# Performance work log

Measured on AMD Instinct MI355X. Metric: run time of the kernel, lower is better.

The kernel has to match this reference:

```python
import jax, jax.numpy as jnp
import numpy as np
from jax import lax

B, S, D, H, FF, STEPS = 8, 1024, 512, 8, 2048, 64
HD = D // H
EPS = 1e-5
NEG_INF = -1e30


def setup_inputs() -> dict:
    key = jax.random.key(0)
    ks = jax.random.split(key, 8)
    sc = 0.02
    inp = {
        "x": jax.random.normal(ks[0], (B, S, D), jnp.float32),
        "decode_x": jax.random.normal(ks[1], (STEPS, B, 1, D), jnp.float32),
        # bool attn mask, True = masked (future positions), matching the torch code
        "causal_mask": jnp.triu(jnp.ones((S, S), bool), k=1),
        "qkv_w": jax.random.normal(ks[2], (3 * D, D), jnp.float32) * sc,
        "qkv_b": jnp.zeros((3 * D,), jnp.float32),
        "out_w": jax.random.normal(ks[3], (D, D), jnp.float32) * sc,
        "out_b": jnp.zeros((D,), jnp.float32),
        "w1": jax.random.normal(ks[4], (FF, D), jnp.float32) * sc,
        "b1": jnp.zeros((FF,), jnp.float32),
        "w2": jax.random.normal(ks[5], (D, FF), jnp.float32) * sc,
        "b2": jnp.zeros((D,), jnp.float32),
        "ln1_w": jnp.ones((D,), jnp.float32),
        "ln1_b": jnp.zeros((D,), jnp.float32),
        "ln2_w": jnp.ones((D,), jnp.float32),
        "ln2_b": jnp.zeros((D,), jnp.float32),
    }
    return inp


def _layer_norm(x, w, b):
    mu = jnp.mean(x, axis=-1, keepdims=True)
    var = jnp.mean(jnp.square(x - mu), axis=-1, keepdims=True)
    return (x - mu) * lax.rsqrt(var + EPS) * w + b


def _mlp(x, w1, b1, w2, b2):
    h = jax.nn.relu(jnp.einsum("bsd,fd->bsf", x, w1) + b1)
    return jnp.einsum("bsf,df->bsd", h, w2) + b2


def _attend(q, k, v, mask):
    # q:[B,H,L,hd] k,v:[B,H,T,hd] mask broadcastable to [B,H,L,T], True = masked
    scale = 1.0 / np.sqrt(HD)
    scores = jnp.einsum("bhld,bhtd->bhlt", q, k) * scale
    scores = jnp.where(mask, NEG_INF, scores)
    w = jax.nn.softmax(scores, axis=-1)
    w = jnp.where(mask, 0.0, w)  # torch code zeros masked weights post-softmax
    return jnp.einsum("bhlt,bhtd->bhld", w, v)


def _heads(t):  # [B,T,D] -> [B,H,T,hd]
    return t.reshape(t.shape[0], t.shape[1], H, HD).transpose(0, 2, 1, 3)


def reference(x, decode_x, causal_mask, qkv_w, qkv_b, out_w, out_b,
              w1, b1, w2, b2, ln1_w, ln1_b, ln2_w, ln2_b):
    # ---- process_prompt (prefill) ----
    qkv = jnp.einsum("bsd,ed->bse", x, qkv_w) + qkv_b  # [B,S,3D]
    q, k, v = jnp.split(qkv, 3, axis=-1)
    attn = _attend(_heads(q), _heads(k), _heads(v), causal_mask[None, None])
    attn = attn.transpose(0, 2, 1, 3).reshape(B, S, D)
    h = x + (jnp.einsum("bsd,ed->bse", attn, out_w) + out_b)
    h = _layer_norm(h, ln1_w, ln1_b)
    h = h + _mlp(h, w1, b1, w2, b2)
    prefill_out = _layer_norm(h, ln2_w, ln2_b)

    cap = S + STEPS
    k_cache = jnp.zeros((B, cap, D), x.dtype).at[:, :S].set(k)
    v_cache = jnp.zeros((B, cap, D), x.dtype).at[:, :S].set(v)
    pos = jnp.arange(cap)

    def step(carry, x_t):
        k_cache, v_cache, cur_len = carry
        qkv = jnp.einsum("bsd,ed->bse", x_t, qkv_w) + qkv_b  # [B,1,3D]
        q, kk, vv = jnp.split(qkv, 3, axis=-1)
        k_cache = lax.dynamic_update_slice(k_cache, kk, (0, cur_len, 0))
        v_cache = lax.dynamic_update_slice(v_cache, vv, (0, cur_len, 0))
        kv_len = cur_len + 1
        mask = (pos >= kv_len)[None, None, None, :]  # [1,1,1,cap]
        attn = _attend(_heads(q), _heads(k_cache), _heads(v_cache), mask)
        attn = attn.transpose(0, 2, 1, 3).reshape(B, 1, D)
        h = x_t + (jnp.einsum("bsd,ed->bse", attn, out_w) + out_b)
        h = _layer_norm(h, ln1_w, ln1_b)
        h = h + _mlp(h, w1, b1, w2, b2)
        h = _layer_norm(h, ln2_w, ln2_b)
        return (k_cache, v_cache, kv_len), h

    (_, _, _), dec = lax.scan(step, (k_cache, v_cache, jnp.int32(S)), decode_x)
    dec = dec.squeeze(2).transpose(1, 0, 2)  # [B,STEPS,D]
    return jnp.concatenate([prefill_out, dec], axis=1)  # [B,S+STEPS,D]
```

## Files before the change

kernel.cpp:

```cpp
#include <hip/hip_runtime.h>
#include <cstdint>

#define CAP_ 1088
#define EPS_ 1e-5f

using bf8   = __attribute__((ext_vector_type(8))) short;
using f32x4 = __attribute__((ext_vector_type(4))) float;

__device__ __forceinline__ unsigned short f2bf(float f) {
  unsigned u = __float_as_uint(f);
  u += 0x7fffu + ((u >> 16) & 1);
  return (unsigned short)(u >> 16);
}

typedef const __attribute__((address_space(1))) void* gp1;
typedef __attribute__((address_space(3))) void* lp3;
__device__ __forceinline__ void async16(const void* g, void* l) {
  __builtin_amdgcn_global_load_lds((gp1)g, (lp3)l, 16, 0, 0);
}

__global__ __launch_bounds__(256) void cvt_bf16(const float* __restrict__ in,
                                                unsigned short* __restrict__ out,
                                                int n4) {
  int i = blockIdx.x * 256 + threadIdx.x;
  if (i >= n4) return;
  float4 v = ((const float4*)in)[i];
  ushort4 o;
  o.x = f2bf(v.x); o.y = f2bf(v.y); o.z = f2bf(v.z); o.w = f2bf(v.w);
  ((ushort4*)out)[i] = o;
}

__global__ __launch_bounds__(256) void mfma_gemm(
    const unsigned short* __restrict__ A, const unsigned short* __restrict__ Bw,
    const float* __restrict__ bias, const float* __restrict__ res,
    const float* __restrict__ res2,
    float* __restrict__ Cf, unsigned short* __restrict__ Cb,
    unsigned short* __restrict__ kb, unsigned short* __restrict__ vt,
    int M, int N, int K, int mode, int relu)
{
  __shared__ unsigned short Als[128 * 64];
  __shared__ unsigned short Bls[128 * 64];
  const int tid  = threadIdx.x;
  const int lane = tid & 63, w = tid >> 6;
  const int bm = blockIdx.x * 128, bn = blockIdx.y * 128;
  const int wm = (w >> 1) * 64, wn = (w & 1) * 64;

  f32x4 acc[4][4] = {};

  const int so = tid * 16;
  for (int k0 = 0; k0 < K; k0 += 64) {
#pragma unroll
    for (int it = 0; it < 4; ++it) {
      int o   = it * 4096 + so;
      int row = o >> 7;
      int ch  = (o >> 4) & 7;
      int sch = ch ^ (row & 7);
      async16(A  + (size_t)(bm + row) * K + k0 + sch * 8, (char*)Als + o);
      async16(Bw + (size_t)(bn + row) * K + k0 + sch * 8, (char*)Bls + o);
    }
    __syncthreads();
#pragma unroll
    for (int ks = 0; ks < 2; ++ks) {
      bf8 af[4], bfr[4];
#pragma unroll
      for (int m = 0; m < 4; ++m) {
        int row = wm + m * 16 + (lane & 15);
        int ch  = ks * 4 + (lane >> 4);
        af[m] = *(const bf8*)((const char*)Als + row * 128 + ((ch ^ (row & 7)) * 16));
      }
#pragma unroll
      for (int n = 0; n < 4; ++n) {
        int row = wn + n * 16 + (lane & 15);
        int ch  = ks * 4 + (lane >> 4);
        bfr[n] = *(const bf8*)((const char*)Bls + row * 128 + ((ch ^ (row & 7)) * 16));
      }
#pragma unroll
      for (int m = 0; m < 4; ++m)
#pragma unroll
        for (int n = 0; n < 4; ++n)
          acc[m][n] = __builtin_amdgcn_mfma_f32_16x16x32_bf16(af[m], bfr[n], acc[m][n], 0, 0, 0);
    }
    __syncthreads();
  }

#pragma unroll
  for (int m = 0; m < 4; ++m) {
#pragma unroll
    for (int n = 0; n < 4; ++n) {
      int col  = bn + wn + n * 16 + (lane & 15);
      int row0 = bm + wm + m * 16 + ((lane >> 4) << 2);
      float bcol = bias[col];
      if (mode == 1) {
        if (col < 512) {
#pragma unroll
          for (int r = 0; r < 4; ++r)
            Cb[((size_t)(row0 + r) << 9) + col] = f2bf((acc[m][n][r] + bcol) * 0.125f);
        } else if (col < 1024) {
#pragma unroll
          for (int r = 0; r < 4; ++r) {
            int row = row0 + r; int bb, pos;
            if (row < 8192) { bb = row >> 10; pos = row & 1023; }
            else { int r2 = row - 8192; bb = r2 & 7; pos = 1024 + (r2 >> 3); }
            kb[(((size_t)(bb * CAP_ + pos)) << 9) + (col - 512)] = f2bf(acc[m][n][r] + bcol);
          }
        } else {
          int c = col - 1024; int hh = c >> 6, d = c & 63;
          if (row0 < 8192) {
            int bb = row0 >> 10, pos = row0 & 1023;
            ushort4 pk;
            pk.x = f2bf(acc[m][n][0] + bcol); pk.y = f2bf(acc[m][n][1] + bcol);
            pk.z = f2bf(acc[m][n][2] + bcol); pk.w = f2bf(acc[m][n][3] + bcol);
            *(ushort4*)(vt + ((size_t)((bb * 8 + hh) * 64 + d)) * CAP_ + pos) = pk;
          } else {
#pragma unroll
            for (int r = 0; r < 4; ++r) {
              int r2 = row0 + r - 8192; int bb = r2 & 7, pos = 1024 + (r2 >> 3);
              vt[((size_t)((bb * 8 + hh) * 64 + d)) * CAP_ + pos] = f2bf(acc[m][n][r] + bcol);
            }
          }
        }
      } else {
#pragma unroll
        for (int r = 0; r < 4; ++r) {
          int row = row0 + r;
          float v = acc[m][n][r] + bcol;
          if (relu) v = fmaxf(v, 0.f);
          if (res) {
            if (res2 && row >= 8192) v += res2[((size_t)(row - 8192) << 9) + col];
            else                     v += res[(size_t)row * N + col];
          }
          if (mode == 0) Cf[(size_t)row * N + col] = v;
          else           Cb[(size_t)row * N + col] = f2bf(v);
        }
      }
    }
  }
}

__global__ __launch_bounds__(256) void attn_mfma(
    const unsigned short* __restrict__ qb,
    const unsigned short* __restrict__ kcb,
    const unsigned short* __restrict__ vtb,
    unsigned short* __restrict__ ob)
{
  __shared__ unsigned short Kls[4096];
  __shared__ unsigned short Vls[4096];
  __shared__ unsigned short Pls[4096];
  const int st = blockIdx.x, bh = blockIdx.y;
  const int b = bh >> 3, h = bh & 7;
  const bool dec = (st == 16);
  const int tid = threadIdx.x, lane = tid & 63, w = tid >> 6;
  const int wq = w * 16;
  const int nT = dec ? 17 : st + 1;
  const int qi = wq + (lane & 15);
  const size_t g = dec ? (size_t)(8192 + qi * 8 + b)
                       : (size_t)((b << 10) + st * 64 + qi);

  const bf8 qf0 = *(const bf8*)(qb + (g << 9) + h * 64 +      ((lane >> 4) << 3));
  const bf8 qf1 = *(const bf8*)(qb + (g << 9) + h * 64 + 32 + ((lane >> 4) << 3));

  f32x4 oo[4] = {};
  float m_ = -1e30f, l_ = 0.f;

  const size_t kbase = (((size_t)b * CAP_) << 9) + h * 64;
  const size_t vbase = (size_t)((b * 8 + h) * 64) * CAP_;

  for (int t = 0; t < nT; ++t) {
    const int t0 = t * 64;
    __syncthreads();
#pragma unroll
    for (int it = 0; it < 2; ++it) {
      int o   = it * 4096 + tid * 16;
      int row = o >> 7;
      int sch = ((o >> 4) & 7) ^ (row & 7);
      async16(kcb + kbase + (((size_t)(t0 + row)) << 9) + sch * 8, (char*)Kls + o);
      async16(vtb + vbase + (size_t)row * CAP_ + t0 + sch * 8,     (char*)Vls + o);
    }
    __syncthreads();

    f32x4 sfr[4] = {};
#pragma unroll
    for (int ks = 0; ks < 2; ++ks) {
      int cb = ks * 4 + (lane >> 4);
      bf8 qv = ks ? qf1 : qf0;
#pragma unroll
      for (int f = 0; f < 4; ++f) {
        int row = f * 16 + (lane & 15);
        bf8 kf = *(const bf8*)((const char*)Kls + row * 128 + ((cb ^ (row & 7)) << 4));
        sfr[f] = __builtin_amdgcn_mfma_f32_16x16x32_bf16(kf, qv, sfr[f], 0, 0, 0);
      }
    }
    if (t == nT - 1) {
#pragma unroll
      for (int f = 0; f < 4; ++f)
#pragma unroll
        for (int r = 0; r < 4; ++r) {
          int tr = f * 16 + ((lane >> 4) << 2) + r;
          if (tr > qi) sfr[f][r] = -1e30f;
        }
    }

    float pmax = -1e30f;
#pragma unroll
    for (int f = 0; f < 4; ++f)
#pragma unroll
      for (int r = 0; r < 4; ++r) pmax = fmaxf(pmax, sfr[f][r]);
    pmax = fmaxf(pmax, __shfl_xor(pmax, 16, 64));
    pmax = fmaxf(pmax, __shfl_xor(pmax, 32, 64));
    float mn  = fmaxf(m_, pmax);
    float fsc = __expf(m_ - mn);
    float rs = 0.f;
#pragma unroll
    for (int f = 0; f < 4; ++f)
#pragma unroll
      for (int r = 0; r < 4; ++r) {
        float e = __expf(sfr[f][r] - mn);
        sfr[f][r] = e; rs += e;
      }
    rs += __shfl_xor(rs, 16, 64);
    rs += __shfl_xor(rs, 32, 64);
    l_ = l_ * fsc + rs; m_ = mn;
#pragma unroll
    for (int f = 0; f < 4; ++f) oo[f] *= fsc;

#pragma unroll
    for (int f = 0; f < 4; ++f) {
      ushort4 pk;
      pk.x = f2bf(sfr[f][0]); pk.y = f2bf(sfr[f][1]);
      pk.z = f2bf(sfr[f][2]); pk.w = f2bf(sfr[f][3]);
      int tb   = f * 32 + ((lane >> 4) << 3);
      int addr = qi * 128 + ((((tb >> 4)) ^ (qi & 7)) << 4) + (tb & 15);
      *(ushort4*)((char*)Pls + addr) = pk;
    }
    __syncthreads();

#pragma unroll
    for (int ks = 0; ks < 2; ++ks) {
      int cb = ks * 4 + (lane >> 4);
      bf8 pf = *(const bf8*)((const char*)Pls + qi * 128 + ((cb ^ (qi & 7)) << 4));
#pragma unroll
      for (int f = 0; f < 4; ++f) {
        int row = f * 16 + (lane & 15);
        bf8 vf = *(const bf8*)((const char*)Vls + row * 128 + ((cb ^ (row & 7)) << 4));
        oo[f] = __builtin_amdgcn_mfma_f32_16x16x32_bf16(vf, pf, oo[f], 0, 0, 0);
      }
    }
  }

  const float inv = 1.f / l_;
#pragma unroll
  for (int f = 0; f < 4; ++f) {
    ushort4 pk;
    pk.x = f2bf(oo[f][0] * inv); pk.y = f2bf(oo[f][1] * inv);
    pk.z = f2bf(oo[f][2] * inv); pk.w = f2bf(oo[f][3] * inv);
    int d0 = f * 16 + ((lane >> 4) << 2);
    *(ushort4*)(ob + (g << 9) + h * 64 + d0) = pk;
  }
}

__global__ __launch_bounds__(256) void ln_rows(
    const float* __restrict__ in, float* __restrict__ outf,
    unsigned short* __restrict__ outb,
    const float* __restrict__ w, const float* __restrict__ bb,
    int outmode)
{
  __shared__ float s1[256], s2[256];
  const int m = blockIdx.x, tid = threadIdx.x;
  const float* row = in + ((size_t)m << 9);
  float x0 = row[tid], x1 = row[tid + 256];
  s1[tid] = x0 + x1;
  s2[tid] = x0 * x0 + x1 * x1;
  __syncthreads();
  for (int st = 128; st > 0; st >>= 1) {
    if (tid < st) { s1[tid] += s1[tid + st]; s2[tid] += s2[tid + st]; }
    __syncthreads();
  }
  float mu  = s1[0] * (1.f / 512.f);
  float var = s2[0] * (1.f / 512.f) - mu * mu;
  float inv = rsqrtf(var + EPS_);
  size_t ob;
  if (outmode == 0) ob = (size_t)m << 9;
  else {
    int b, s;
    if (m < 8192) { b = m >> 10; s = m & 1023; }
    else { int r2 = m - 8192; b = r2 & 7; s = 1024 + (r2 >> 3); }
    ob = ((size_t)(b * CAP_ + s)) << 9;
  }
  float y0 = (x0 - mu) * inv * w[tid] + bb[tid];
  float y1 = (x1 - mu) * inv * w[tid + 256] + bb[tid + 256];
  outf[ob + tid] = y0; outf[ob + tid + 256] = y1;
  if (outb) {
    outb[((size_t)m << 9) + tid]       = f2bf(y0);
    outb[((size_t)m << 9) + tid + 256] = f2bf(y1);
  }
}

extern "C" void kernel_launch(void* const* d_in, const int* in_sizes, int n_in,
                              void* d_out, int out_size, void* d_ws, size_t ws_size,
                              hipStream_t stream)
{
  const float* x     = (const float*)d_in[0];
  const float* dx    = (const float*)d_in[1];
  const float* qkv_w = (const float*)d_in[3];
  const float* qkv_b = (const float*)d_in[4];
  const float* out_w = (const float*)d_in[5];
  const float* out_b = (const float*)d_in[6];
  const float* w1    = (const float*)d_in[7];
  const float* b1    = (const float*)d_in[8];
  const float* w2    = (const float*)d_in[9];
  const float* b2    = (const float*)d_in[10];
  const float* ln1w  = (const float*)d_in[11];
  const float* ln1b  = (const float*)d_in[12];
  const float* ln2w  = (const float*)d_in[13];
  const float* ln2b  = (const float*)d_in[14];
  float* out = (float*)d_out;

  float* ws = (float*)d_ws;
  size_t o = 0;
  unsigned short* x_bf    = (unsigned short*)(ws + o); o += (size_t)8704 * 256;
  unsigned short* qkvw_bf = (unsigned short*)(ws + o); o += 1536 * 256;
  unsigned short* outw_bf = (unsigned short*)(ws + o); o += 512 * 256;
  unsigned short* w1_bf   = (unsigned short*)(ws + o); o += 2048 * 256;
  unsigned short* w2_bf   = (unsigned short*)(ws + o); o += (size_t)512 * 1024;
  unsigned short* qb_bf   = (unsigned short*)(ws + o); o += (size_t)8704 * 256;
  unsigned short* kcb     = (unsigned short*)(ws + o); o += (size_t)8 * CAP_ * 256;
  unsigned short* vtb     = (unsigned short*)(ws + o); o += (size_t)8 * 512 * CAP_ / 2;
  unsigned short* attn_bf = (unsigned short*)(ws + o); o += (size_t)8704 * 256;
  float* h                = ws + o;                    o += (size_t)8704 * 512;
  unsigned short* h_bf    = (unsigned short*)(ws + o); o += (size_t)8704 * 256;
  unsigned short* hid_bf  = (unsigned short*)(ws + o); o += (size_t)8704 * 1024;
  float* h2               = ws + o;                    o += (size_t)8704 * 512;

  cvt_bf16<<<dim3(4096), 256, 0, stream>>>(x,  x_bf,                      1048576);
  cvt_bf16<<<dim3(256),  256, 0, stream>>>(dx, x_bf + (size_t)8192 * 512, 65536);
  cvt_bf16<<<dim3(768),  256, 0, stream>>>(qkv_w, qkvw_bf, 196608);
  cvt_bf16<<<dim3(256),  256, 0, stream>>>(out_w, outw_bf, 65536);
  cvt_bf16<<<dim3(1024), 256, 0, stream>>>(w1,    w1_bf,   262144);
  cvt_bf16<<<dim3(1024), 256, 0, stream>>>(w2,    w2_bf,   262144);

  mfma_gemm<<<dim3(68, 12), 256, 0, stream>>>(x_bf, qkvw_bf, qkv_b, nullptr, nullptr,
      nullptr, qb_bf, kcb, vtb, 8704, 1536, 512, 1, 0);
  attn_mfma<<<dim3(17, 64), 256, 0, stream>>>(qb_bf, kcb, vtb, attn_bf);
  mfma_gemm<<<dim3(68, 4), 256, 0, stream>>>(attn_bf, outw_bf, out_b, x, dx,
      h, nullptr, nullptr, nullptr, 8704, 512, 512, 0, 0);
  ln_rows<<<dim3(8704), 256, 0, stream>>>(h, h, h_bf, ln1w, ln1b, 0);
  mfma_gemm<<<dim3(68, 16), 256, 0, stream>>>(h_bf, w1_bf, b1, nullptr, nullptr,
      nullptr, hid_bf, nullptr, nullptr, 8704, 2048, 512, 2, 1);
  mfma_gemm<<<dim3(68, 4), 256, 0, stream>>>(hid_bf, w2_bf, b2, h, nullptr,
      h2, nullptr, nullptr, nullptr, 8704, 512, 2048, 0, 0);
  ln_rows<<<dim3(8704), 256, 0, stream>>>(h2, out, nullptr, ln2w, ln2b, 5);
}
```

Before: 350.1 us.

## Fuse residual add and LayerNorm into full-row output-projection and FFN2 GEMMs

Adds a GEMM kernel where each block computes 32 full rows of 512 outputs, so bias, residual add and LayerNorm run in the epilogue, replacing the separate ln_rows launches and fp32 intermediates. Residuals are now read from bf16 copies (x_bf, h1_bf) rather than fp32, which cuts memory traffic but lowers the precision of the residual path. The new kernel uses 272 blocks with 64KB LDS and no double buffering of B, so it may get less parallelism than the previous 68x4 tiling.

```diff
diff --git a/kernel.cpp b/kernel.cpp
--- a/kernel.cpp
+++ b/kernel.cpp
@@ -11,6 +11,9 @@
   unsigned u = __float_as_uint(f);
   u += 0x7fffu + ((u >> 16) & 1);
   return (unsigned short)(u >> 16);
+}
+__device__ __forceinline__ float bf2f(unsigned short v) {
+  return __uint_as_float((unsigned)v << 16);
 }
 
 typedef const __attribute__((address_space(1))) void* gp1;
@@ -32,9 +35,8 @@
 
 __global__ __launch_bounds__(256) void mfma_gemm(
     const unsigned short* __restrict__ A, const unsigned short* __restrict__ Bw,
-    const float* __restrict__ bias, const float* __restrict__ res,
-    const float* __restrict__ res2,
-    float* __restrict__ Cf, unsigned short* __restrict__ Cb,
+    const float* __restrict__ bias,
+    unsigned short* __restrict__ Cb,
     unsigned short* __restrict__ kb, unsigned short* __restrict__ vt,
     int M, int N, int K, int mode, int relu)
 {
@@ -122,19 +124,143 @@
       } else {
 #pragma unroll
         for (int r = 0; r < 4; ++r) {
-          int row = row0 + r;
           float v = acc[m][n][r] + bcol;
           if (relu) v = fmaxf(v, 0.f);
-          if (res) {
-            if (res2 && row >= 8192) v += res2[((size_t)(row - 8192) << 9) + col];
-            else                     v += res[(size_t)row * N + col];
-          }
-          if (mode == 0) Cf[(size_t)row * N + col] = v;
-          else           Cb[(size_t)row * N + col] = f2bf(v);
+          Cb[(size_t)(row0 + r) * N + col] = f2bf(v);
         }
       }
     }
   }
+}
+
+__global__ __launch_bounds__(256) void gemm_fullrow_ln(
+    const unsigned short* __restrict__ A,
+    const unsigned short* __restrict__ Bw,
+    const float* __restrict__ bias,
+    const unsigned short* __restrict__ resb,
+    const float* __restrict__ lnw, const float* __restrict__ lnb,
+    unsigned short* __restrict__ outb, float* __restrict__ outf,
+    int K, int mode)
+{
+  __shared__ unsigned short Bls[512 * 64];
+  const int tid = threadIdx.x, lane = tid & 63, w = tid >> 6;
+  const int l4 = lane >> 4, l15 = lane & 15;
+  const int bm = blockIdx.x * 32;
+
+  f32x4 acc[2][8] = {};
+  bf8 a_cur[2][2], a_nxt[2][2];
+
+#pragma unroll
+  for (int ks = 0; ks < 2; ++ks)
+#pragma unroll
+    for (int mf = 0; mf < 2; ++mf)
+      a_cur[ks][mf] = *(const bf8*)(A + (size_t)(bm + mf * 16 + l15) * K + (ks * 4 + l4) * 8);
+
+  for (int k0 = 0; k0 < K; k0 += 64) {
+#pragma unroll
+    for (int it = 0; it < 16; ++it) {
+      int o   = it * 4096 + tid * 16;
+      int row = o >> 7;
+      int sch = ((o >> 4) & 7) ^ (row & 7);
+      async16(Bw + (size_t)row * K + k0 + sch * 8, (char*)Bls + o);
+    }
+    if (k0 + 64 < K) {
+#pragma unroll
+      for (int ks = 0; ks < 2; ++ks)
+#pragma unroll
+        for (int mf = 0; mf < 2; ++mf)
+          a_nxt[ks][mf] = *(const bf8*)(A + (size_t)(bm + mf * 16 + l15) * K +
+                                        k0 + 64 + (ks * 4 + l4) * 8);
+    }
+    __syncthreads();
+#pragma unroll
+    for (int ks = 0; ks < 2; ++ks) {
+      int cb = ks * 4 + l4;
+#pragma unroll
+      for (int nf = 0; nf < 8; ++nf) {
+        int row = w * 128 + nf * 16 + l15;
+        bf8 bfv = *(const bf8*)((const char*)Bls + row * 128 + ((cb ^ (row & 7)) << 4));
+#pragma unroll
+        for (int mf = 0; mf < 2; ++mf)
+          acc[mf][nf] = __builtin_amdgcn_mfma_f32_16x16x32_bf16(a_cur[ks][mf], bfv, acc[mf][nf], 0, 0, 0);
+      }
+    }
+#pragma unroll
+    for (int ks = 0; ks < 2; ++ks)
+#pragma unroll
+      for (int mf = 0; mf < 2; ++mf)
+        a_cur[ks][mf] = a_nxt[ks][mf];
+    __syncthreads();
+  }
+
+  float bc[8], lw[8], lb[8];
+#pragma unroll
+  for (int nf = 0; nf < 8; ++nf) {
+    int col = w * 128 + nf * 16 + l15;
+    bc[nf] = bias[col]; lw[nf] = lnw[col]; lb[nf] = lnb[col];
+  }
+#pragma unroll
+  for (int nf = 0; nf < 8; ++nf) {
+    int col = w * 128 + nf * 16 + l15;
+#pragma unroll
+    for (int mf = 0; mf < 2; ++mf)
+#pragma unroll
+      for (int r = 0; r < 4; ++r) {
+        int rowg = bm + mf * 16 + l4 * 4 + r;
+        acc[mf][nf][r] += bc[nf] + bf2f(resb[(size_t)rowg * 512 + col]);
+      }
+  }
+
+  float* red = (float*)Bls;
+#pragma unroll
+  for (int mf = 0; mf < 2; ++mf)
+#pragma unroll
+    for (int r = 0; r < 4; ++r) {
+      float s = 0.f, q = 0.f;
+#pragma unroll
+      for (int nf = 0; nf < 8; ++nf) { float v = acc[mf][nf][r]; s += v; q += v * v; }
+#pragma unroll
+      for (int off = 1; off < 16; off <<= 1) {
+        s += __shfl_xor(s, off, 64); q += __shfl_xor(q, off, 64);
+      }
+      if (l15 == 0) {
+        int rl = mf * 16 + l4 * 4 + r;
+        red[rl * 8 + w * 2]     = s;
+        red[rl * 8 + w * 2 + 1] = q;
+      }
+    }
+  __syncthreads();
+
+#pragma unroll
+  for (int mf = 0; mf < 2; ++mf)
+#pragma unroll
+    for (int r = 0; r < 4; ++r) {
+      int rl = mf * 16 + l4 * 4 + r;
+      float S = red[rl * 8 + 0] + red[rl * 8 + 2] + red[rl * 8 + 4] + red[rl * 8 + 6];
+      float Q = red[rl * 8 + 1] + red[rl * 8 + 3] + red[rl * 8 + 5] + red[rl * 8 + 7];
+      float mu  = S * (1.f / 512.f);
+      float var = Q * (1.f / 512.f) - mu * mu;
+      float inv = rsqrtf(var + EPS_);
+      int rowg = bm + rl;
+      if (mode == 0) {
+#pragma unroll
+        for (int nf = 0; nf < 8; ++nf) {
+          int col = w * 128 + nf * 16 + l15;
+          float y = (acc[mf][nf][r] - mu) * inv * lw[nf] + lb[nf];
+          outb[(size_t)rowg * 512 + col] = f2bf(y);
+        }
+      } else {
+        int b, s2;
+        if (rowg < 8192) { b = rowg >> 10; s2 = rowg & 1023; }
+        else { int r2 = rowg - 8192; b = r2 & 7; s2 = 1024 + (r2 >> 3); }
+        size_t ob = ((size_t)(b * CAP_ + s2)) << 9;
+#pragma unroll
+        for (int nf = 0; nf < 8; ++nf) {
+          int col = w * 128 + nf * 16 + l15;
+          outf[ob + col] = (acc[mf][nf][r] - mu) * inv * lw[nf] + lb[nf];
+        }
+      }
+    }
 }
 
 __global__ __launch_bounds__(256) void attn_mfma(
@@ -255,43 +381,6 @@
     pk.z = f2bf(oo[f][2] * inv); pk.w = f2bf(oo[f][3] * inv);
     int d0 = f * 16 + ((lane >> 4) << 2);
     *(ushort4*)(ob + (g << 9) + h * 64 + d0) = pk;
-  }
-}
-
-__global__ __launch_bounds__(256) void ln_rows(
-    const float* __restrict__ in, float* __restrict__ outf,
-    unsigned short* __restrict__ outb,
-    const float* __restrict__ w, const float* __restrict__ bb,
-    int outmode)
-{
-  __shared__ float s1[256], s2[256];
-  const int m = blockIdx.x, tid = threadIdx.x;
-  const float* row = in + ((size_t)m << 9);
-  float x0 = row[tid], x1 = row[tid + 256];
-  s1[tid] = x0 + x1;
-  s2[tid] = x0 * x0 + x1 * x1;
-  __syncthreads();
-  for (int st = 128; st > 0; st >>= 1) {
-    if (tid < st) { s1[tid] += s1[tid + st]; s2[tid] += s2[tid + st]; }
-    __syncthreads();
-  }
-  float mu  = s1[0] * (1.f / 512.f);
-  float var = s2[0] * (1.f / 512.f) - mu * mu;
-  float inv = rsqrtf(var + EPS_);
-  size_t ob;
-  if (outmode == 0) ob = (size_t)m << 9;
-  else {
-    int b, s;
-    if (m < 8192) { b = m >> 10; s = m & 1023; }
-    else { int r2 = m - 8192; b = r2 & 7; s = 1024 + (r2 >> 3); }
-    ob = ((size_t)(b * CAP_ + s)) << 9;
-  }
-  float y0 = (x0 - mu) * inv * w[tid] + bb[tid];
-  float y1 = (x1 - mu) * inv * w[tid + 256] + bb[tid + 256];
-  outf[ob + tid] = y0; outf[ob + tid + 256] = y1;
-  if (outb) {
-    outb[((size_t)m << 9) + tid]       = f2bf(y0);
-    outb[((size_t)m << 9) + tid + 256] = f2bf(y1);
   }
 }
 
@@ -326,10 +415,8 @@
   unsigned short* kcb     = (unsigned short*)(ws + o); o += (size_t)8 * CAP_ * 256;
   unsigned short* vtb     = (unsigned short*)(ws + o); o += (size_t)8 * 512 * CAP_ / 2;
   unsigned short* attn_bf = (unsigned short*)(ws + o); o += (size_t)8704 * 256;
-  float* h                = ws + o;                    o += (size_t)8704 * 512;
-  unsigned short* h_bf    = (unsigned short*)(ws + o); o += (size_t)8704 * 256;
+  unsigned short* h1_bf   = (unsigned short*)(ws + o); o += (size_t)8704 * 256;
   unsigned short* hid_bf  = (unsigned short*)(ws + o); o += (size_t)8704 * 1024;
-  float* h2               = ws + o;                    o += (size_t)8704 * 512;
 
   cvt_bf16<<<dim3(4096), 256, 0, stream>>>(x,  x_bf,                      1048576);
   cvt_bf16<<<dim3(256),  256, 0, stream>>>(dx, x_bf + (size_t)8192 * 512, 65536);
@@ -338,15 +425,13 @@
   cvt_bf16<<<dim3(1024), 256, 0, stream>>>(w1,    w1_bf,   262144);
   cvt_bf16<<<dim3(1024), 256, 0, stream>>>(w2,    w2_bf,   262144);
 
-  mfma_gemm<<<dim3(68, 12), 256, 0, stream>>>(x_bf, qkvw_bf, qkv_b, nullptr, nullptr,
-      nullptr, qb_bf, kcb, vtb, 8704, 1536, 512, 1, 0);
+  mfma_gemm<<<dim3(68, 12), 256, 0, stream>>>(x_bf, qkvw_bf, qkv_b,
+      qb_bf, kcb, vtb, 8704, 1536, 512, 1, 0);
   attn_mfma<<<dim3(17, 64), 256, 0, stream>>>(qb_bf, kcb, vtb, attn_bf);
-  mfma_gemm<<<dim3(68, 4), 256, 0, stream>>>(attn_bf, outw_bf, out_b, x, dx,
-      h, nullptr, nullptr, nullptr, 8704, 512, 512, 0, 0);
-  ln_rows<<<dim3(8704), 256, 0, stream>>>(h, h, h_bf, ln1w, ln1b, 0);
-  mfma_gemm<<<dim3(68, 16), 256, 0, stream>>>(h_bf, w1_bf, b1, nullptr, nullptr,
-      nullptr, hid_bf, nullptr, nullptr, 8704, 2048, 512, 2, 1);
-  mfma_gemm<<<dim3(68, 4), 256, 0, stream>>>(hid_bf, w2_bf, b2, h, nullptr,
-      h2, nullptr, nullptr, nullptr, 8704, 512, 2048, 0, 0);
-  ln_rows<<<dim3(8704), 256, 0, stream>>>(h2, out, nullptr, ln2w, ln2b, 5);
-}
+  gemm_fullrow_ln<<<dim3(272), 256, 0, stream>>>(attn_bf, outw_bf, out_b,
+      x_bf, ln1w, ln1b, h1_bf, nullptr, 512, 0);
+  mfma_gemm<<<dim3(68, 16), 256, 0, stream>>>(h1_bf, w1_bf, b1,
+      hid_bf, nullptr, nullptr, 8704, 2048, 512, 2, 1);
+  gemm_fullrow_ln<<<dim3(272), 256, 0, stream>>>(hid_bf, w2_bf, b2,
+      h1_bf, ln2w, ln2b, nullptr, out, 2048, 1);
+}
```

Result: faster. 310.5 us (-11.3%).
